# Performance work log

Measured on AMD Instinct MI355X. Metric: run time of the kernel, lower is better.

## Reference

```python
import jax, jax.numpy as jnp
import numpy as np

B = 128   # batch_size (number of trees / source tweets)
H = 100   # tweet_out_size == GRU hidden == GAT feature dim


def _gru_layer(x, h0, Wih, Whh, bih, bhh):
    # x: [T, N, D] time-major; PyTorch GRU cell math
    def step(h, xt):
        gi = xt @ Wih.T + bih
        gh = h @ Whh.T + bhh
        ir, iz, in_ = jnp.split(gi, 3, axis=-1)
        hr, hz, hn = jnp.split(gh, 3, axis=-1)
        r = jax.nn.sigmoid(ir + hr)
        z = jax.nn.sigmoid(iz + hz)
        n = jnp.tanh(in_ + r * hn)
        h = (1.0 - z) * n + z * h
        return h, h
    hT, ys = jax.lax.scan(step, h0, x)
    return ys, hT


def _gru2(x, h0, Wih0, Whh0, bih0, bhh0, Wih1, Whh1, bih1, bhh1):
    y0, _ = _gru_layer(x, h0[0], Wih0, Whh0, bih0, bhh0)
    _, h1 = _gru_layer(y0, h0[1], Wih1, Whh1, bih1, bhh1)
    return h1  # final hidden of top layer: [N, H]


def _gat(x, ei, W, a_src, a_dst, b, heads, outc, concat):
    # PyG GATConv (eval mode, add_self_loops=True, leaky_relu slope 0.2)
    N = x.shape[0]
    loops = jnp.arange(N, dtype=ei.dtype)
    src = jnp.concatenate([ei[0], loops])
    dst = jnp.concatenate([ei[1], loops])
    h = (x @ W.T).reshape(N, heads, outc)           # [N, H, C]
    es = (h * a_src).sum(-1)                         # [N, H]
    ed = (h * a_dst).sum(-1)
    e = jax.nn.leaky_relu(es[src] + ed[dst], negative_slope=0.2)  # [E, H]
    m = jax.lax.stop_gradient(jax.ops.segment_max(e, dst, num_segments=N))
    ee = jnp.exp(e - m[dst])
    s = jax.ops.segment_sum(ee, dst, num_segments=N)
    alpha = ee / s[dst]
    out = jax.ops.segment_sum(h[src] * alpha[:, :, None], dst, num_segments=N)
    out = out.reshape(N, heads * outc) if concat else out.mean(axis=1)
    return out + b


def _forward(fl, user_text, gnode, gei, tnode, tei, idx):
    (user_feats, h0g, h0t, temb,
     gWih0, gWhh0, gbih0, gbhh0, gWih1, gWhh1, gbih1, gbhh1,
     tWih0, tWhh0, tbih0, tbhh0, tWih1, tWhh1, tbih1, tbhh1,
     uW1, ub1, uW2, ub2,
     gc1W, gc1as, gc1ad, gc1b, gc2W, gc2as, gc2ad, gc2b,
     tc1W, tc1as, tc1ad, tc1b, tc2W, tc2as, tc2ad, tc2b,
     fcW, fcb) = fl
    # --- graphGAT branch ---
    ue = jax.nn.relu(user_feats @ uW1.T + ub1) @ uW2.T + ub2        # [Nu, 100]
    ge = temb[gnode].transpose(1, 0, 2)                              # [T, Ntg, 100]
    hg = _gru2(ge, h0g, gWih0, gWhh0, gbih0, gbhh0, gWih1, gWhh1, gbih1, gbhh1)
    xg = jnp.concatenate([hg[:B], ue, hg[B:]], axis=0)               # [Ng, 100]
    xg = jax.nn.relu(_gat(xg, gei, gc1W, gc1as, gc1ad, gc1b, 8, 64, True))
    xg = jax.nn.relu(_gat(xg, gei, gc2W, gc2as, gc2ad, gc2b, 1, 100, False))
    # --- TreeGAT branch ---
    te = temb[tnode].transpose(1, 0, 2)                              # [T, Ntree, 100]
    ht = _gru2(te, h0t, tWih0, tWhh0, tbih0, tbhh0, tWih1, tWhh1, tbih1, tbhh1)
    xt = ht.at[:B].set(xg[:B])                                       # root rows <- user_root_embed
    xt = jax.nn.relu(_gat(xt, tei, tc1W, tc1as, tc1ad, tc1b, 8, 100, True))
    xt = jax.nn.relu(_gat(xt, tei, tc2W, tc2as, tc2ad, tc2b, 1, 100, False))
    # --- scatter_mean over trees + classifier ---
    ssum = jax.ops.segment_sum(xt, idx, num_segments=B)
    cnt = jax.ops.segment_sum(jnp.ones((xt.shape[0],), xt.dtype), idx, num_segments=B)
    mean = ssum / jnp.maximum(cnt, 1.0)[:, None]
    return mean @ fcW.T + fcb                                        # [B, 4]


def setup_inputs():
    key = jax.random.key(0)
    it = iter(jax.random.split(key, 60))
    def nrm(shape, s):
        return (jax.random.normal(next(it), shape) * s).astype(jnp.float32)
    Ntg, Nu, Ntree = 10000, 20000, 30000
    Ng = Ntg + Nu
    Eg, Et, V, T = 200000, 60000, 50000, 20
    inp = {}
    inp["user_text"] = jax.random.randint(next(it), (Nu, 10), 0, 1000)
    inp["user_feats"] = nrm((Nu, 9), 1.0)
    inp["graph_node_features"] = jax.random.randint(next(it), (Ntg, T), 0, V)
    inp["graph_edge_index"] = jax.random.randint(next(it), (2, Eg), 0, Ng)
    inp["merged_tree_feature"] = jax.random.randint(next(it), (Ntree, T), 0, V)
    inp["merged_tree_edge_index"] = jax.random.randint(next(it), (2, Et), 0, Ntree)
    inp["indices"] = jax.random.randint(next(it), (Ntree,), 0, B)
    inp["h0_graph"] = nrm((2, Ntg, H), 1.0)
    inp["h0_tree"] = nrm((2, Ntree, H), 1.0)
    inp["tweet_emb"] = nrm((V, H), 1.0)
    s = 0.1
    for p in ("g", "t"):
        for l in ("0", "1"):
            inp[p + "Wih" + l] = nrm((3 * H, H), s)
            inp[p + "Whh" + l] = nrm((3 * H, H), s)
            inp[p + "bih" + l] = jnp.zeros((3 * H,), jnp.float32)
            inp[p + "bhh" + l] = jnp.zeros((3 * H,), jnp.float32)
    inp["uW1"] = nrm((100, 9), s);    inp["ub1"] = jnp.zeros((100,), jnp.float32)
    inp["uW2"] = nrm((100, 100), s);  inp["ub2"] = jnp.zeros((100,), jnp.float32)
    inp["gc1W"] = nrm((512, 100), s); inp["gc1as"] = nrm((8, 64), s); inp["gc1ad"] = nrm((8, 64), s); inp["gc1b"] = jnp.zeros((512,), jnp.float32)
    inp["gc2W"] = nrm((100, 512), s); inp["gc2as"] = nrm((1, 100), s); inp["gc2ad"] = nrm((1, 100), s); inp["gc2b"] = jnp.zeros((100,), jnp.float32)
    inp["tc1W"] = nrm((800, 100), s); inp["tc1as"] = nrm((8, 100), s); inp["tc1ad"] = nrm((8, 100), s); inp["tc1b"] = jnp.zeros((800,), jnp.float32)
    inp["tc2W"] = nrm((100, 800), s); inp["tc2as"] = nrm((1, 100), s); inp["tc2ad"] = nrm((1, 100), s); inp["tc2b"] = jnp.zeros((100,), jnp.float32)
    inp["fcW"] = nrm((4, 100), s);    inp["fcb"] = jnp.zeros((4,), jnp.float32)
    return inp


def reference(user_text, user_feats, graph_node_features, graph_edge_index,
              merged_tree_feature, merged_tree_edge_index, indices,
              h0_graph, h0_tree, tweet_emb,
              gWih0, gWhh0, gbih0, gbhh0, gWih1, gWhh1, gbih1, gbhh1,
              tWih0, tWhh0, tbih0, tbhh0, tWih1, tWhh1, tbih1, tbhh1,
              uW1, ub1, uW2, ub2,
              gc1W, gc1as, gc1ad, gc1b, gc2W, gc2as, gc2ad, gc2b,
              tc1W, tc1as, tc1ad, tc1b, tc2W, tc2as, tc2ad, tc2b,
              fcW, fcb):
    fl = (user_feats, h0_graph, h0_tree, tweet_emb,
          gWih0, gWhh0, gbih0, gbhh0, gWih1, gWhh1, gbih1, gbhh1,
          tWih0, tWhh0, tbih0, tbhh0, tWih1, tWhh1, tbih1, tbhh1,
          uW1, ub1, uW2, ub2,
          gc1W, gc1as, gc1ad, gc1b, gc2W, gc2as, gc2ad, gc2b,
          tc1W, tc1as, tc1ad, tc1b, tc2W, tc2as, tc2ad, tc2b,
          fcW, fcb)
    return _forward(fl, user_text, graph_node_features, graph_edge_index,
                    merged_tree_feature, merged_tree_edge_index, indices)
```

## Files before the change

### kernel.cpp

```cpp
#include <hip/hip_runtime.h>

#define NB    128
#define HD    100
#define NU    20000
#define NTG   10000
#define NTREE 30000
#define NG    30000
#define TT    20
#define EG    200000
#define ET    60000
#define VOC   50000

#define ESTR2 448
#define WROWS 336
#define LOG2E  1.4426950408889634f
#define LOG2E2 2.8853900817779268f

typedef unsigned short u16;
typedef unsigned int   u32;
typedef __attribute__((ext_vector_type(8))) short short8;
typedef __attribute__((ext_vector_type(4))) float floatx4;

__device__ __forceinline__ float sigmoid2_(float y) {
    return __fdividef(1.f, 1.f + __builtin_amdgcn_exp2f(-y));
}
__device__ __forceinline__ float tanh2_(float y) {
    return 1.f - __fdividef(2.f, __builtin_amdgcn_exp2f(y) + 1.f);
}
__device__ __forceinline__ u16 f2bf(float f) {
    u32 u = __float_as_uint(f);
    u32 r = (u + 0x7fffu + ((u >> 16) & 1u)) >> 16;
    return (u16)r;
}
__device__ __forceinline__ u16 f2bf_c(float f) {
    u32 r;
    asm("v_cvt_pk_bf16_f32 %0, %1, %2" : "=v"(r) : "v"(f), "v"(f));
    return (u16)r;
}
__device__ __forceinline__ float bf2f(u16 h) {
    return __uint_as_float(((u32)h) << 16);
}

struct GruProb {
    const u16*   Etab;
    const int*   nodes;
    const float* h0;
    const u16*   Whh0;
    const u16*   Wih1;
    const u16*   Whh1;
    u16*         hout;
    int          M;
};

__global__ __launch_bounds__(448, 2) void gru_fused10(GruProb Pg, GruProb Pt, int gblocks)
{
    const bool isg = (int)blockIdx.x < gblocks;
    const GruProb P = isg ? Pg : Pt;
    const int bx = isg ? blockIdx.x : blockIdx.x - gblocks;
    const int M  = P.M;
    const int m0 = bx * 32;

    __shared__ u16 H0[2][32 * 128];
    __shared__ u16 H1[2][32 * 128];
    __shared__ int NID[TT * 32];

    const int tid  = threadIdx.x;
    const int w    = tid >> 6, lane = tid & 63;
    const int fr   = lane & 15, quad = lane >> 4;
    const int c    = w * 16 + fr;
    const bool cok = (c < HD);

    short8 Bh0[3][4], Bx1[3][4], Bh1[3][4];
#pragma unroll
    for (int g = 0; g < 3; ++g) {
        const size_t rb = (size_t)((g * 7 + w) * 16 + fr) * 128 + quad * 8;
#pragma unroll
        for (int kk = 0; kk < 4; ++kk) {
            Bh0[g][kk] = *(const short8*)(P.Whh0 + rb + kk * 32);
            Bx1[g][kk] = *(const short8*)(P.Wih1 + rb + kk * 32);
            Bh1[g][kk] = *(const short8*)(P.Whh1 + rb + kk * 32);
        }
    }

    for (int i = tid; i < 32 * 128; i += 448) {
        H0[0][i] = 0; H0[1][i] = 0; H1[0][i] = 0; H1[1][i] = 0;
    }
    for (int i = tid; i < 32 * TT; i += 448) {
        int row = i / TT, t = i - row * TT;
        int gm = m0 + row;
        NID[t * 32 + row] = (gm < M) ? P.nodes[(size_t)gm * TT + t] : 0;
    }
    __syncthreads();
    if (tid < 32) {
        int off = 200 ^ ((tid & 7) << 4);
        *(u16*)((char*)&H0[0][0] + tid * 256 + off) = 0x3F80;
        *(u16*)((char*)&H0[1][0] + tid * 256 + off) = 0x3F80;
        *(u16*)((char*)&H1[0][0] + tid * 256 + off) = 0x3F80;
// ... 254 lines not shown
            acc[t] = __builtin_amdgcn_mfma_f32_16x16x32_bf16(af, bf, acc[t], 0, 0, 0);
        }
    }

    const int orow0 = m0 + (wave << 4) + quad * 4;
#pragma unroll
    for (int t = 0; t < 4; ++t) {
        int col = n0 + (t << 4) + fr;
        if (col >= N) continue;
#pragma unroll
        for (int r = 0; r < 4; ++r)
            Cb[(size_t)(orow0 + r) * ESTR2 + col] = f2bf(acc[t][r]);
    }
}

__global__ __launch_bounds__(256) void gemm_nt(
    const float* __restrict__ A, const float* __restrict__ W,
    const float* __restrict__ bias, float* __restrict__ C,
    int M, int N, int K, int relu)
{
    const int m0 = blockIdx.x * 64;
    const int n0 = blockIdx.y * 64;
    __shared__ float As[20][68];
    __shared__ float Ws[20][68];
    const int tid = threadIdx.x;
    const int r0 = (tid >> 4) * 4;
    const int c0 = (tid & 15) * 4;
    int sr[5], sk[5];
#pragma unroll
    for (int it = 0; it < 5; ++it) {
        int idx = tid + it * 256;
        sr[it] = idx / 20; sk[it] = idx - sr[it] * 20;
    }
    float acc[4][4];
#pragma unroll
    for (int i = 0; i < 4; ++i)
#pragma unroll
        for (int j = 0; j < 4; ++j) acc[i][j] = 0.f;
    const int nch = (K + 19) / 20;
    for (int ch = 0; ch < nch; ++ch) {
        const int k0 = ch * 20;
#pragma unroll
        for (int it = 0; it < 5; ++it) {
            int m = m0 + sr[it], k = k0 + sk[it];
            float va = 0.f, vw = 0.f;
            if (k < K) {
                if (m < M) va = A[(size_t)m * K + k];
                int n = n0 + sr[it];
                if (n < N) vw = W[(size_t)n * K + k];
            }
            As[sk[it]][sr[it]] = va;
            Ws[sk[it]][sr[it]] = vw;
        }
        __syncthreads();
#pragma unroll
        for (int kkk = 0; kkk < 20; ++kkk) {
            float4 a = *(const float4*)&As[kkk][r0];
            float4 w = *(const float4*)&Ws[kkk][c0];
            float av[4] = {a.x, a.y, a.z, a.w};
            float wv[4] = {w.x, w.y, w.z, w.w};
#pragma unroll
            for (int i = 0; i < 4; ++i)
#pragma unroll
                for (int j = 0; j < 4; ++j)
                    acc[i][j] = fmaf(av[i], wv[j], acc[i][j]);
        }
        __syncthreads();
    }
#pragma unroll
    for (int i = 0; i < 4; ++i) {
        int m = m0 + r0 + i;
        if (m >= M) continue;
#pragma unroll
        for (int j = 0; j < 4; ++j) {
            int n = n0 + c0 + j;
            if (n >= N) continue;
            float v = acc[i][j] + (bias ? bias[n] : 0.f);
            if (relu) v = fmaxf(v, 0.f);
            C[(size_t)m * N + n] = v;
        }
    }
}

__global__ void convert_pad2(const float* __restrict__ src, u16* __restrict__ dst,
                             int M, int Mp, int K, int ldk,
                             const float* __restrict__ app, int appone)
{
    int t = blockIdx.x * blockDim.x + threadIdx.x;
    if (t >= Mp * ldk) return;
    int n = t / ldk, c = t - n * ldk;
    u16 o = 0;
    if (n < M) {
        if (c < K) o = f2bf(src[(size_t)n * K + c]);
        else if (c == 100) {
            if (app) o = f2bf(app[n]);
            else if (appone) o = 0x3F80;
        }
    }
    dst[t] = o;
}

struct CvtgBatch {
    const float* src[6];
    const float* bias[6];
    u16*         dst[6];
};
#define CVTG_BLOCKS_PER_MAT 168
__global__ void convert_gru_w6(CvtgBatch B)
{
    int mat = blockIdx.x / CVTG_BLOCKS_PER_MAT;
    int t = (blockIdx.x - mat * CVTG_BLOCKS_PER_MAT) * blockDim.x + threadIdx.x;
    int rr = t >> 7, cc = t & 127;
    int g = rr / 112, r2 = rr - g * 112;
    u16 o = 0;
    if (r2 < 100) {
        float sc = (g == 2) ? LOG2E2 : LOG2E;
        int sr = g * 100 + r2;
        if (cc < 100) o = f2bf(B.src[mat][(size_t)sr * 100 + cc] * sc);
        else if (cc == 100) o = f2bf(B.bias[mat][sr] * sc);
    }
    B.dst[mat][t] = o;
}

__global__ void convert_ih0(const float* __restrict__ s0, const float* __restrict__ b0,
                            u16* __restrict__ d0,
                            const float* __restrict__ s1, const float* __restrict__ b1,
                            u16* __restrict__ d1)
{
    int t = blockIdx.x * blockDim.x + threadIdx.x;
    if (t >= 2 * 448 * 128) return;
    int which = t / (448 * 128);
    int tt = t - which * (448 * 128);
    const float* s = which ? s1 : s0;
    const float* b = which ? b1 : b0;
    u16* d = which ? d1 : d0;
    int j = tt >> 7, kc = tt & 127;
    int cc = j >> 2, g = j & 3;
    u16 o = 0;
    if (g < 3 && cc < 100) {
        float sc = (g == 2) ? LOG2E2 : LOG2E;
        int sr = g * 100 + cc;
        if (kc < 100) o = f2bf(s[(size_t)sr * 100 + kc] * sc);
        else if (kc == 100) o = f2bf(b[sr] * sc);
    }
    d[tt] = o;
}

__global__ void build_xg_bf(const u16* __restrict__ hgb, const float* __restrict__ ue,
                            u16* __restrict__ xgb)
{
    int t = blockIdx.x * blockDim.x + threadIdx.x;
    if (t >= NG * 128) return;
    int n = t >> 7, c = t & 127;
    u16 o = 0;
    if (n < NB)           o = hgb[n * 128 + c];
    else if (n < NB + NU) { if (c < HD) o = f2bf(ue[(size_t)(n - NB) * HD + c]); }
    else                  o = hgb[(size_t)(n - NU) * 128 + c];
    xgb[t] = o;
}

__global__ void set_roots(const float* __restrict__ src, u16* __restrict__ hb)
{
    int t = blockIdx.x * blockDim.x + threadIdx.x;
    if (t >= NB * HD) return;
    int n = t / HD, c = t - n * HD;
    hb[(size_t)n * 128 + c] = f2bf(src[t]);
}

__global__ void csr_count2(const int* __restrict__ gei, const int* __restrict__ tei,
                           int* __restrict__ gcnt, int* __restrict__ tcnt)
{
    int e = blockIdx.x * blockDim.x + threadIdx.x;
    const int GE = EG + NG;
    if (e < GE) {
        int dst = (e < EG) ? gei[EG + e] : e - EG;
        atomicAdd(&gcnt[dst], 1);
    } else {
        int e2 = e - GE;
        if (e2 >= ET + NTREE) return;
        int dst = (e2 < ET) ? tei[ET + e2] : e2 - ET;
        atomicAdd(&tcnt[dst], 1);
    }
}

__global__ void csr_scan2(int* __restrict__ gcnt, int* __restrict__ goff, int* __restrict__ gcur,
                          int* __restrict__ tcnt, int* __restrict__ toff, int* __restrict__ tcur)
{
    const int* cnt = blockIdx.x ? tcnt : gcnt;
    int* off = blockIdx.x ? toff : goff;
    int* cur = blockIdx.x ? tcur : gcur;
    const int N = blockIdx.x ? NTREE : NG;
    __shared__ int part[256];
    const int tid = threadIdx.x;
    const int per = (N + 255) / 256;
    const int i0 = tid * per;
    const int i1 = min(i0 + per, N);
    int s = 0;
    for (int i = i0; i < i1; ++i) s += cnt[i];
    part[tid] = s;
    __syncthreads();
    for (int o = 1; o < 256; o <<= 1) {
        int u = (tid >= o) ? part[tid - o] : 0;
        __syncthreads();
        part[tid] += u;
        __syncthreads();
    }
    int base = part[tid] - s;
    for (int i = i0; i < i1; ++i) {
        off[i] = base; cur[i] = base;
        base += cnt[i];
    }
    if (tid == 255) off[N] = part[255];
}

__global__ void csr_scatter2(const int* __restrict__ gei, const int* __restrict__ tei,
                             int* __restrict__ gcur, int* __restrict__ tcur,
                             int* __restrict__ geidx, int* __restrict__ teidx)
{
    int e = blockIdx.x * blockDim.x + threadIdx.x;
    const int GE = EG + NG;
    if (e < GE) {
        int dst = (e < EG) ? gei[EG + e] : e - EG;
        int pos = atomicAdd(&gcur[dst], 1);
        geidx[pos] = e;
    } else {
        int e2 = e - GE;
        if (e2 >= ET + NTREE) return;
        int dst = (e2 < ET) ? tei[ET + e2] : e2 - ET;
        int pos = atomicAdd(&tcur[dst], 1);
        teidx[pos] = e2;
    }
}

__global__ void gat_es_ed(const u16* __restrict__ feat, const float* __restrict__ asrc,
                          const float* __restrict__ adst, float* __restrict__ es,
                          float* __restrict__ ed, int N, int heads, int C)
{
    int gid = blockIdx.x * blockDim.x + threadIdx.x;
    if (gid >= N * heads) return;
    int n = gid / heads, hd = gid - n * heads;
    const u16* hp = feat + ((size_t)n * heads + hd) * C;
    const float* as = asrc + (size_t)hd * C;
    const float* ad = adst + (size_t)hd * C;
    float s1 = 0.f, s2 = 0.f;
    for (int c = 0; c < C; c += 4) {
        uint2 pk = *(const uint2*)(hp + c);
        float v0 = bf2f((u16)(pk.x & 0xffff)), v1 = bf2f((u16)(pk.x >> 16));
        float v2 = bf2f((u16)(pk.y & 0xffff)), v3 = bf2f((u16)(pk.y >> 16));
        s1 += v0 * as[c] + v1 * as[c + 1] + v2 * as[c + 2] + v3 * as[c + 3];
        s2 += v0 * ad[c] + v1 * ad[c + 1] + v2 * ad[c + 2] + v3 * ad[c + 3];
    }
    es[gid] = s1; ed[gid] = s2;
}

template<int HEADS>
__global__ __launch_bounds__(256) void gat_alpha_csr(
    const int* __restrict__ off, const int* __restrict__ eidx,
    const int* __restrict__ ei, int E,
    const float* __restrict__ es, const float* __restrict__ ed,
    float* __restrict__ eb, int N)
{
    int gt = blockIdx.x * blockDim.x + threadIdx.x;
    int dst = gt >> 6, lane = gt & 63;
    if (dst >= N) return;
    const int hd  = lane & (HEADS - 1);
    const int esl = lane / HEADS;
    const int EPI = 64 / HEADS;
    const int e0 = off[dst], e1 = off[dst + 1];
    const float edv = ed[(size_t)dst * HEADS + hd];

    float mymax = -3.4e38f;
    for (int p0 = e0; p0 < e1; p0 += EPI) {
        int p = p0 + esl;
        if (p < e1) {
            int j = eidx[p];
            int src = (j < E) ? ei[j] : (j - E);
            float e = es[(size_t)src * HEADS + hd] + edv;
            e = e > 0.f ? e : 0.2f * e;
            mymax = fmaxf(mymax, e);
        }
    }
#pragma unroll
    for (int o = HEADS; o < 64; o <<= 1)
        mymax = fmaxf(mymax, __shfl_xor(mymax, o));

    float ssum = 0.f;
    for (int p0 = e0; p0 < e1; p0 += EPI) {
        int p = p0 + esl;
        if (p < e1) {
            int j = eidx[p];
            int src = (j < E) ? ei[j] : (j - E);
            float e = es[(size_t)src * HEADS + hd] + edv;
            e = e > 0.f ? e : 0.2f * e;
            ssum += __expf(e - mymax);
        }
    }
#pragma unroll
    for (int o = HEADS; o < 64; o <<= 1)
        ssum += __shfl_xor(ssum, o);
    float sinv = __fdividef(1.f, ssum);

    for (int p0 = e0; p0 < e1; p0 += EPI) {
        int p = p0 + esl;
        if (p < e1) {
            int j = eidx[p];
            int src = (j < E) ? ei[j] : (j - E);
            float e = es[(size_t)src * HEADS + hd] + edv;
            e = e > 0.f ? e : 0.2f * e;
            eb[(size_t)j * HEADS + hd] = __expf(e - mymax) * sinv;
        }
    }
}

template<int C, int VEC>
__global__ __launch_bounds__(256) void gat_accum_csr(
    const int* __restrict__ off, const int* __restrict__ eidx,
    const int* __restrict__ ei, int E,
    const float* __restrict__ eb,
    const u16* __restrict__ feat, const float* __restrict__ bias,
    float* __restrict__ outf, u16* __restrict__ outb,
    int N, int heads, int HC, int nchunk)
{
    int gt = blockIdx.x * blockDim.x + threadIdx.x;
    int w = gt >> 6, lane = gt & 63;
    int dst = w / nchunk, chunk = w - dst * nchunk;
    if (dst >= N) return;
    int c0 = chunk * 64 * VEC + lane * VEC;
    if (c0 >= HC) return;
    int hh[VEC]; float acc[VEC];
#pragma unroll
    for (int v = 0; v < VEC; ++v) {
        int c = c0 + v;
        hh[v] = c / C;
        acc[v] = 0.f;
    }
    int e0 = off[dst], e1 = off[dst + 1];
    for (int p = e0; p < e1; ++p) {
        int j = eidx[p];
        int src = (j < E) ? ei[j] : (j - E);
        const u16* frp = feat + (size_t)src * HC + c0;
        float fv[VEC];
        if (VEC == 8) {
            uint4 pk = *(const uint4*)frp;
            fv[0] = bf2f((u16)(pk.x & 0xffff)); fv[1] = bf2f((u16)(pk.x >> 16));
            fv[2] = bf2f((u16)(pk.y & 0xffff)); fv[3] = bf2f((u16)(pk.y >> 16));
            fv[4] = bf2f((u16)(pk.z & 0xffff)); fv[5] = bf2f((u16)(pk.z >> 16));
            fv[6] = bf2f((u16)(pk.w & 0xffff)); fv[7] = bf2f((u16)(pk.w >> 16));
        } else if (VEC == 4) {
            uint2 pk = *(const uint2*)frp;
            fv[0] = bf2f((u16)(pk.x & 0xffff)); fv[1] = bf2f((u16)(pk.x >> 16));
            fv[2] = bf2f((u16)(pk.y & 0xffff)); fv[3] = bf2f((u16)(pk.y >> 16));
        } else {
            u32 pk = *(const u32*)frp;
            fv[0] = bf2f((u16)(pk & 0xffff)); fv[1] = bf2f((u16)(pk >> 16));
        }
#pragma unroll
        for (int v = 0; v < VEC; ++v)
            acc[v] += fv[v] * eb[(size_t)j * heads + hh[v]];
    }
#pragma unroll
    for (int v = 0; v < VEC; ++v) {
        int c = c0 + v;
        if (c >= HC) continue;
        float o = fmaxf(acc[v] + bias[c], 0.f);
        if (outf) outf[(size_t)dst * HC + c] = o;
        if (outb) outb[(size_t)dst * HC + c] = f2bf(o);
    }
}

__global__ void scatter_mean_accum(const float* __restrict__ x, const int* __restrict__ idx,
                                   float* __restrict__ ssum, float* __restrict__ cnt)
{
    int t = blockIdx.x * blockDim.x + threadIdx.x;
    if (t >= NTREE * HD) return;
    int n = t / HD, c = t - n * HD;
    int b = idx[n];
    atomicAdd(&ssum[b * HD + c], x[t]);
    if (c == 0) atomicAdd(&cnt[b], 1.f);
}

__global__ void fc_out(const float* __restrict__ ssum, const float* __restrict__ cnt,
                       const float* __restrict__ W, const float* __restrict__ b,
                       float* __restrict__ out)
{
    int t = threadIdx.x;
    int bb = t >> 2, j = t & 3;
    float inv = __fdividef(1.f, fmaxf(cnt[bb], 1.f));
    float acc = b[j];
    for (int k = 0; k < HD; ++k) acc += ssum[bb * HD + k] * inv * W[j * HD + k];
    out[t] = acc;
}

extern "C" void kernel_launch(void* const* d_in, const int* in_sizes, int n_in,
                              void* d_out, int out_size, void* d_ws, size_t ws_size,
                              hipStream_t stream)
{
    const float* user_feats = (const float*)d_in[1];
    const int*   gnf        = (const int*)d_in[2];
    const int*   gei        = (const int*)d_in[3];
    const int*   tnf        = (const int*)d_in[4];
    const int*   tei        = (const int*)d_in[5];
    const int*   indices    = (const int*)d_in[6];
    const float* h0g        = (const float*)d_in[7];
    const float* h0t        = (const float*)d_in[8];
    const float* temb       = (const float*)d_in[9];
    const float* gW[2][4] = {{(const float*)d_in[10], (const float*)d_in[11], (const float*)d_in[12], (const float*)d_in[13]},
                             {(const float*)d_in[14], (const float*)d_in[15], (const float*)d_in[16], (const float*)d_in[17]}};
    const float* tW[2][4] = {{(const float*)d_in[18], (const float*)d_in[19], (const float*)d_in[20], (const float*)d_in[21]},
                             {(const float*)d_in[22], (const float*)d_in[23], (const float*)d_in[24], (const float*)d_in[25]}};
    const float* uW1 = (const float*)d_in[26]; const float* ub1 = (const float*)d_in[27];
    const float* uW2 = (const float*)d_in[28]; const float* ub2 = (const float*)d_in[29];
    const float* gc1W = (const float*)d_in[30]; const float* gc1as = (const float*)d_in[31];
    const float* gc1ad = (const float*)d_in[32]; const float* gc1b = (const float*)d_in[33];
    const float* gc2W = (const float*)d_in[34]; const float* gc2as = (const float*)d_in[35];
    const float* gc2ad = (const float*)d_in[36]; const float* gc2b = (const float*)d_in[37];
    const float* tc1W = (const float*)d_in[38]; const float* tc1as = (const float*)d_in[39];
    const float* tc1ad = (const float*)d_in[40]; const float* tc1b = (const float*)d_in[41];
    const float* tc2W = (const float*)d_in[42]; const float* tc2as = (const float*)d_in[43];
    const float* tc2ad = (const float*)d_in[44]; const float* tc2b = (const float*)d_in[45];
    const float* fcW = (const float*)d_in[46]; const float* fcb = (const float*)d_in[47];
    float* out = (float*)d_out;

    char* ws = (char*)d_ws;
    const size_t NEED = 226500000;
    if (ws_size < NEED) return;

    float* XGF    = (float*)(ws + 0);
    u16*   TEMB_B = (u16*)(ws + 12000000);
    u16*   ETAB_G = (u16*)(ws + 25000000);
    u16*   ETAB_T = (u16*)(ws + 70000000);
    u16*   GH1B   = (u16*)(ws + 115000000);
    u16*   TH1B   = (u16*)(ws + 117600000);
    float* UE     = (float*)(ws + 125300000);
    float* HID    = (float*)(ws + 133400000);
    u16*   WARENA = (u16*)(ws + 141500000);
    int*   GOFF   = (int*)(ws + 142700000);
    int*   GCUR   = (int*)(ws + 142900000);
    int*   GCNT   = (int*)(ws + 143100000);
    int*   TCNT   = (int*)(ws + 143220000);
    int*   GEIDX  = (int*)(ws + 143400000);
    int*   TOFF   = (int*)(ws + 144400000);
    int*   TCUR   = (int*)(ws + 144600000);
    int*   TEIDX  = (int*)(ws + 144800000);
    float* ESB    = (float*)(ws + 145300000);
    float* EDB    = (float*)(ws + 146300000);
    float* EBB    = (float*)(ws + 149300000);
    float* SSUM   = (float*)(ws + 156700000);
    float* SCNT   = (float*)(ws + 156800000);
    u16*   XG_B   = (u16*)(ws + 157000000);
    u16*   GFEAT1 = (u16*)(ws + 165000000);
    u16*   GOUT1B = (u16*)(ws + 25000000);
    u16*   GFEAT2 = (u16*)(ws + 56000000);
    u16*   TFEAT1 = (u16*)(ws + 25000000);
    u16*   TOUT1B = (u16*)(ws + 74000000);
    u16*   TFEAT2 = (u16*)(ws + 123000000);
    float* XOUT2  = (float*)(ws + 157000000);

    u16* gWHH0  = WARENA + 0;
    u16* gWIH1  = WARENA + 43008;
    u16* gWHH1  = WARENA + 86016;
    u16* tWHH0  = WARENA + 129024;
    u16* tWIH1  = WARENA + 172032;
    u16* tWHH1  = WARENA + 215040;
    u16* W_IH0A = WARENA + 258048;
    u16* W_IH0B = WARENA + 315392;
    u16* W_G1   = WARENA + 372736;
    u16* W_G2   = WARENA + 475136;

    auto cvt = [&](const float* src, u16* dst, int M, int Mp, int K, int ldk,
                   const float* app = nullptr, int appone = 0) {
        convert_pad2<<<((size_t)Mp * ldk + 255) / 256, 256, 0, stream>>>(
            src, dst, M, Mp, K, ldk, app, appone);
    };
    auto mfma = [&](const u16* A, int lda, const u16* W, int ldw,
                    float* Cf, u16* Cb, int ldc, int M, int N, int Kt) {
        dim3 grid((M + 63) / 64, (N + 63) / 64, 1);
        gemm_mfma<<<grid, 256, 0, stream>>>(A, W, Cf, Cb, M, N, Kt, lda, ldw, ldc);
    };

    {
        dim3 g1((NU + 63) / 64, (HD + 63) / 64, 1);
        gemm_nt<<<g1, 256, 0, stream>>>(user_feats, uW1, ub1, HID, NU, HD, 9, 1);
        gemm_nt<<<g1, 256, 0, stream>>>(HID, uW2, ub2, UE, NU, HD, HD, 0);
    }

    cvt(temb, TEMB_B, VOC, VOC, HD, 128, nullptr, 1);
    {
        CvtgBatch B;
        B.src[0] = gW[0][1]; B.bias[0] = gW[0][3]; B.dst[0] = gWHH0;
        B.src[1] = gW[1][0]; B.bias[1] = gW[1][2]; B.dst[1] = gWIH1;
        B.src[2] = gW[1][1]; B.bias[2] = gW[1][3]; B.dst[2] = gWHH1;
        B.src[3] = tW[0][1]; B.bias[3] = tW[0][3]; B.dst[3] = tWHH0;
        B.src[4] = tW[1][0]; B.bias[4] = tW[1][2]; B.dst[4] = tWIH1;
        B.src[5] = tW[1][1]; B.bias[5] = tW[1][3]; B.dst[5] = tWHH1;
        convert_gru_w6<<<6 * CVTG_BLOCKS_PER_MAT, 256, 0, stream>>>(B);
    }
    convert_ih0<<<(2 * 448 * 128 + 255) / 256, 256, 0, stream>>>(
        gW[0][0], gW[0][2], W_IH0A, tW[0][0], tW[0][2], W_IH0B);
    {
        dim3 ge((VOC + 63) / 64, 7, 2);
        gemm_etab<<<ge, 256, 0, stream>>>(TEMB_B, W_IH0A, W_IH0B, ETAB_G, ETAB_T);
    }

    hipMemsetAsync(GCNT, 0, 143400000 - 143100000, stream);
    {
        int tot = (EG + NG) + (ET + NTREE);
        csr_count2<<<(tot + 255) / 256, 256, 0, stream>>>(gei, tei, GCNT, TCNT);
        csr_scan2<<<2, 256, 0, stream>>>(GCNT, GOFF, GCUR, TCNT, TOFF, TCUR);
        csr_scatter2<<<(tot + 255) / 256, 256, 0, stream>>>(gei, tei, GCUR, TCUR, GEIDX, TEIDX);
    }

    {
        GruProb Pg = { ETAB_G, gnf, h0g, gWHH0, gWIH1, gWHH1, GH1B, NTG };
        GruProb Pt = { ETAB_T, tnf, h0t, tWHH0, tWIH1, tWHH1, TH1B, NTREE };
        int gblk = (NTG + 31) / 32;
        int tblk = (NTREE + 31) / 32;
        gru_fused10<<<gblk + tblk, 448, 0, stream>>>(Pg, Pt, gblk);
    }

    build_xg_bf<<<(NG * 128 + 255) / 256, 256, 0, stream>>>(GH1B, UE, XG_B);
    cvt(gc1W, W_G1, 512, 512, HD, 128);
    cvt(gc2W, W_G2, 100, 100, 512, 512);
    {
        mfma(XG_B, 128, W_G1, 128, nullptr, GFEAT1, 512, NG, 512, 4);
        gat_es_ed<<<(NG * 8 + 255) / 256, 256, 0, stream>>>(GFEAT1, gc1as, gc1ad, ESB, EDB, NG, 8, 64);
        gat_alpha_csr<8><<<(NG + 3) / 4, 256, 0, stream>>>(GOFF, GEIDX, gei, EG, ESB, EDB, EBB, NG);
        gat_accum_csr<64, 8><<<(NG + 3) / 4, 256, 0, stream>>>(
            GOFF, GEIDX, gei, EG, EBB, GFEAT1, gc1b, nullptr, GOUT1B, NG, 8, 512, 1);
    }
    {
        mfma(GOUT1B, 512, W_G2, 512, nullptr, GFEAT2, 100, NG, 100, 16);
        gat_es_ed<<<(NG + 255) / 256, 256, 0, stream>>>(GFEAT2, gc2as, gc2ad, ESB, EDB, NG, 1, 100);
        gat_alpha_csr<1><<<(NG + 3) / 4, 256, 0, stream>>>(GOFF, GEIDX, gei, EG, ESB, EDB, EBB, NG);
        gat_accum_csr<100, 2><<<(NG + 3) / 4, 256, 0, stream>>>(
            GOFF, GEIDX, gei, EG, EBB, GFEAT2, gc2b, XGF, nullptr, NG, 1, 100, 1);
    }

    set_roots<<<(NB * HD + 255) / 256, 256, 0, stream>>>(XGF, TH1B);
    cvt(tc1W, W_G1, 800, 800, HD, 128);
    cvt(tc2W, W_G2, 100, 100, 800, 800);
    {
        mfma(TH1B, 128, W_G1, 128, nullptr, TFEAT1, 800, NTREE, 800, 4);
        gat_es_ed<<<(NTREE * 8 + 255) / 256, 256, 0, stream>>>(TFEAT1, tc1as, tc1ad, ESB, EDB, NTREE, 8, 100);
        gat_alpha_csr<8><<<(NTREE + 3) / 4, 256, 0, stream>>>(TOFF, TEIDX, tei, ET, ESB, EDB, EBB, NTREE);
        gat_accum_csr<100, 8><<<(NTREE * 2 + 3) / 4, 256, 0, stream>>>(
            TOFF, TEIDX, tei, ET, EBB, TFEAT1, tc1b, nullptr, TOUT1B, NTREE, 8, 800, 2);
    }
    {
        mfma(TOUT1B, 800, W_G2, 800, nullptr, TFEAT2, 100, NTREE, 100, 25);
        gat_es_ed<<<(NTREE + 255) / 256, 256, 0, stream>>>(TFEAT2, tc2as, tc2ad, ESB, EDB, NTREE, 1, 100);
        gat_alpha_csr<1><<<(NTREE + 3) / 4, 256, 0, stream>>>(TOFF, TEIDX, tei, ET, ESB, EDB, EBB, NTREE);
        gat_accum_csr<100, 2><<<(NTREE + 3) / 4, 256, 0, stream>>>(
            TOFF, TEIDX, tei, ET, EBB, TFEAT2, tc2b, XOUT2, nullptr, NTREE, 1, 100, 1);
    }

    hipMemsetAsync(SSUM, 0, (size_t)NB * HD * 4, stream);
    hipMemsetAsync(SCNT, 0, (size_t)NB * 4, stream);
    scatter_mean_accum<<<(NTREE * HD + 255) / 256, 256, 0, stream>>>(XOUT2, indices, SSUM, SCNT);
    fc_out<<<1, 512, 0, stream>>>(SSUM, SCNT, fcW, fcb, out);
}
```

Before: 1.485 ms.

## Fuse GAT alpha into aggregation, batch weight conversions, CSR-based scatter mean

```diff
diff --git a/kernel.cpp b/kernel.cpp
--- a/kernel.cpp
+++ b/kernel.cpp
@@ -12,7 +12,6 @@
 #define VOC   50000
 
 #define ESTR2 448
-#define WROWS 336
 #define LOG2E  1.4426950408889634f
 #define LOG2E2 2.8853900817779268f
 
@@ -433,68 +432,74 @@
     }
 }
 
-__global__ void convert_pad2(const float* __restrict__ src, u16* __restrict__ dst,
-                             int M, int Mp, int K, int ldk,
-                             const float* __restrict__ app, int appone)
-{
-    int t = blockIdx.x * blockDim.x + threadIdx.x;
-    if (t >= Mp * ldk) return;
+struct CvtAll {
+    const float* temb;  u16* tembB;
+    const float* gsrc[6]; const float* gbias[6]; u16* gdst[6];
+    const float* is[2];   const float* ib[2];    u16* id_[2];
+    const float* wsrc[4]; u16* wdst[4];
+    int wK[4]; int wLdk[4]; int wTot[4];
+};
+#define CB_TEMB 25000
+#define CB_GRUW 168
+#define CB_IH0  224
+#define CB_WTOT 1169
+
+__global__ void convert_all(CvtAll P)
+{
+    int b = blockIdx.x;
+    const int tid = threadIdx.x;
+    if (b < CB_TEMB) {
+        int t = b * 256 + tid;
+        int n = t >> 7, c = t & 127;
+        u16 o = 0;
+        if (c < 100) o = f2bf(P.temb[(size_t)n * 100 + c]);
+        else if (c == 100) o = 0x3F80;
+        P.tembB[t] = o;
+        return;
+    }
+    b -= CB_TEMB;
+    if (b < 6 * CB_GRUW) {
+        int mat = b / CB_GRUW;
+        int t = (b - mat * CB_GRUW) * 256 + tid;
+        int rr = t >> 7, cc = t & 127;
+        int g = rr / 112, r2 = rr - g * 112;
+        u16 o = 0;
+        if (r2 < 100) {
+            float sc = (g == 2) ? LOG2E2 : LOG2E;
+            int sr = g * 100 + r2;
+            if (cc < 100) o = f2bf(P.gsrc[mat][(size_t)sr * 100 + cc] * sc);
+            else if (cc == 100) o = f2bf(P.gbias[mat][sr] * sc);
+        }
+        P.gdst[mat][t] = o;
+        return;
+    }
+    b -= 6 * CB_GRUW;
+    if (b < 2 * CB_IH0) {
+        int which = b / CB_IH0;
+        int t = (b - which * CB_IH0) * 256 + tid;
+        int j = t >> 7, kc = t & 127;
+        int cc = j >> 2, g = j & 3;
+        u16 o = 0;
+        if (g < 3 && cc < 100) {
+            float sc = (g == 2) ? LOG2E2 : LOG2E;
+            int sr = g * 100 + cc;
+            if (kc < 100) o = f2bf(P.is[which][(size_t)sr * 100 + kc] * sc);
+            else if (kc == 100) o = f2bf(P.ib[which][sr] * sc);
+        }
+        P.id_[which][t] = o;
+        return;
+    }
+    b -= 2 * CB_IH0;
+    int seg, t;
+    if (b < 256)      { seg = 0; t = b * 256 + tid; }
+    else if (b < 456) { seg = 1; t = (b - 256) * 256 + tid; }
+    else if (b < 856) { seg = 2; t = (b - 456) * 256 + tid; }
+    else              { seg = 3; t = (b - 856) * 256 + tid; }
+    if (t >= P.wTot[seg]) return;
+    int K = P.wK[seg], ldk = P.wLdk[seg];
     int n = t / ldk, c = t - n * ldk;
-    u16 o = 0;
-    if (n < M) {
-        if (c < K) o = f2bf(src[(size_t)n * K + c]);
-        else if (c == 100) {
-            if (app) o = f2bf(app[n]);
-            else if (appone) o = 0x3F80;
-        }
-    }
-    dst[t] = o;
-}
-
-struct CvtgBatch {
-    const float* src[6];
-    const float* bias[6];
-    u16*         dst[6];
-};
-#define CVTG_BLOCKS_PER_MAT 168
-__global__ void convert_gru_w6(CvtgBatch B)
-{
-    int mat = blockIdx.x / CVTG_BLOCKS_PER_MAT;
-    int t = (blockIdx.x - mat * CVTG_BLOCKS_PER_MAT) * blockDim.x + threadIdx.x;
-    int rr = t >> 7, cc = t & 127;
-    int g = rr / 112, r2 = rr - g * 112;
-    u16 o = 0;
-    if (r2 < 100) {
-        float sc = (g == 2) ? LOG2E2 : LOG2E;
-        int sr = g * 100 + r2;
-        if (cc < 100) o = f2bf(B.src[mat][(size_t)sr * 100 + cc] * sc);
-        else if (cc == 100) o = f2bf(B.bias[mat][sr] * sc);
-    }
-    B.dst[mat][t] = o;
-}
-
-__global__ void convert_ih0(const float* __restrict__ s0, const float* __restrict__ b0,
-                            u16* __restrict__ d0,
-                            const float* __restrict__ s1, const float* __restrict__ b1,
-                            u16* __restrict__ d1)
-{
-    int t = blockIdx.x * blockDim.x + threadIdx.x;
-    if (t >= 2 * 448 * 128) return;
-    int which = t / (448 * 128);
-    int tt = t - which * (448 * 128);
-    const float* s = which ? s1 : s0;
-    const float* b = which ? b1 : b0;
-    u16* d = which ? d1 : d0;
-    int j = tt >> 7, kc = tt & 127;
-    int cc = j >> 2, g = j & 3;
-    u16 o = 0;
-    if (g < 3 && cc < 100) {
-        float sc = (g == 2) ? LOG2E2 : LOG2E;
-        int sr = g * 100 + cc;
-        if (kc < 100) o = f2bf(s[(size_t)sr * 100 + kc] * sc);
-        else if (kc == 100) o = f2bf(b[sr] * sc);
-    }
-    d[tt] = o;
+    u16 o = (c < K) ? f2bf(P.wsrc[seg][(size_t)n * K + c]) : (u16)0;
+    P.wdst[seg][t] = o;
 }
 
 __global__ void build_xg_bf(const u16* __restrict__ hgb, const float* __restrict__ ue,
@@ -519,28 +524,34 @@
 }
 
 __global__ void csr_count2(const int* __restrict__ gei, const int* __restrict__ tei,
-                           int* __restrict__ gcnt, int* __restrict__ tcnt)
+                           const int* __restrict__ bmap,
+                           int* __restrict__ gcnt, int* __restrict__ tcnt,
+                           int* __restrict__ bcnt)
 {
     int e = blockIdx.x * blockDim.x + threadIdx.x;
-    const int GE = EG + NG;
+    const int GE = EG + NG, TE = ET + NTREE;
     if (e < GE) {
         int dst = (e < EG) ? gei[EG + e] : e - EG;
         atomicAdd(&gcnt[dst], 1);
-    } else {
+    } else if (e < GE + TE) {
         int e2 = e - GE;
-        if (e2 >= ET + NTREE) return;
         int dst = (e2 < ET) ? tei[ET + e2] : e2 - ET;
         atomicAdd(&tcnt[dst], 1);
+    } else {
+        int e3 = e - GE - TE;
+        if (e3 >= NTREE) return;
+        atomicAdd(&bcnt[bmap[e3]], 1);
     }
 }
 
 __global__ void csr_scan2(int* __restrict__ gcnt, int* __restrict__ goff, int* __restrict__ gcur,
-                          int* __restrict__ tcnt, int* __restrict__ toff, int* __restrict__ tcur)
-{
-    const int* cnt = blockIdx.x ? tcnt : gcnt;
-    int* off = blockIdx.x ? toff : goff;
-    int* cur = blockIdx.x ? tcur : gcur;
-    const int N = blockIdx.x ? NTREE : NG;
+                          int* __restrict__ tcnt, int* __restrict__ toff, int* __restrict__ tcur,
+                          int* __restrict__ bcnt, int* __restrict__ boff, int* __restrict__ bcur)
+{
+    const int* cnt; int* off; int* cur; int N;
+    if (blockIdx.x == 0)      { cnt = gcnt; off = goff; cur = gcur; N = NG; }
+    else if (blockIdx.x == 1) { cnt = tcnt; off = toff; cur = tcur; N = NTREE; }
+    else                      { cnt = bcnt; off = boff; cur = bcur; N = NB; }
     __shared__ int part[256];
     const int tid = threadIdx.x;
     const int per = (N + 255) / 256;
@@ -565,21 +576,28 @@
 }
 
 __global__ void csr_scatter2(const int* __restrict__ gei, const int* __restrict__ tei,
+                             const int* __restrict__ bmap,
                              int* __restrict__ gcur, int* __restrict__ tcur,
-                             int* __restrict__ geidx, int* __restrict__ teidx)
+                             int* __restrict__ bcur,
+                             int* __restrict__ geidx, int* __restrict__ teidx,
+                             int* __restrict__ bidx)
 {
     int e = blockIdx.x * blockDim.x + threadIdx.x;
-    const int GE = EG + NG;
+    const int GE = EG + NG, TE = ET + NTREE;
     if (e < GE) {
         int dst = (e < EG) ? gei[EG + e] : e - EG;
         int pos = atomicAdd(&gcur[dst], 1);
         geidx[pos] = e;
-    } else {
+    } else if (e < GE + TE) {
         int e2 = e - GE;
-        if (e2 >= ET + NTREE) return;
         int dst = (e2 < ET) ? tei[ET + e2] : e2 - ET;
         int pos = atomicAdd(&tcur[dst], 1);
         teidx[pos] = e2;
+    } else {
+        int e3 = e - GE - TE;
+        if (e3 >= NTREE) return;
+        int pos = atomicAdd(&bcur[bmap[e3]], 1);
+        bidx[pos] = e3;
     }
 }
 
@@ -604,91 +622,75 @@
     es[gid] = s1; ed[gid] = s2;
 }
 
-template<int HEADS>
-__global__ __launch_bounds__(256) void gat_alpha_csr(
+template<int C, int VEC, int HEADS, int NCHUNK>
+__global__ __launch_bounds__(256) void gat_fused(
     const int* __restrict__ off, const int* __restrict__ eidx,
     const int* __restrict__ ei, int E,
     const float* __restrict__ es, const float* __restrict__ ed,
-    float* __restrict__ eb, int N)
+    const u16* __restrict__ feat, const float* __restrict__ bias,
+    float* __restrict__ outf, u16* __restrict__ outb,
+    int N, int HC)
 {
     int gt = blockIdx.x * blockDim.x + threadIdx.x;
-    int dst = gt >> 6, lane = gt & 63;
+    int wid = gt >> 6, lane = gt & 63;
+    int dst = wid / NCHUNK, chunk = wid - dst * NCHUNK;
     if (dst >= N) return;
+    const int e0 = off[dst], e1 = off[dst + 1];
+
     const int hd  = lane & (HEADS - 1);
     const int esl = lane / HEADS;
     const int EPI = 64 / HEADS;
-    const int e0 = off[dst], e1 = off[dst + 1];
-    const float edv = ed[(size_t)dst * HEADS + hd];
+    float edv = ed[(size_t)dst * HEADS + hd];
 
     float mymax = -3.4e38f;
-    for (int p0 = e0; p0 < e1; p0 += EPI) {
-        int p = p0 + esl;
-        if (p < e1) {
-            int j = eidx[p];
-            int src = (j < E) ? ei[j] : (j - E);
-            float e = es[(size_t)src * HEADS + hd] + edv;
-            e = e > 0.f ? e : 0.2f * e;
-            mymax = fmaxf(mymax, e);
-        }
+    for (int p = e0 + esl; p < e1; p += EPI) {
+        int j = eidx[p];
+        int src = (j < E) ? ei[j] : (j - E);
+        float e = es[(size_t)src * HEADS + hd] + edv;
+        e = e > 0.f ? e : 0.2f * e;
+        mymax = fmaxf(mymax, e);
     }
 #pragma unroll
     for (int o = HEADS; o < 64; o <<= 1)
         mymax = fmaxf(mymax, __shfl_xor(mymax, o));
 
     float ssum = 0.f;
-    for (int p0 = e0; p0 < e1; p0 += EPI) {
-        int p = p0 + esl;
-        if (p < e1) {
-            int j = eidx[p];
-            int src = (j < E) ? ei[j] : (j - E);
-            float e = es[(size_t)src * HEADS + hd] + edv;
-            e = e > 0.f ? e : 0.2f * e;
-            ssum += __expf(e - mymax);
-        }
+    for (int p = e0 + esl; p < e1; p += EPI) {
+        int j = eidx[p];
+        int src = (j < E) ? ei[j] : (j - E);
+        float e = es[(size_t)src * HEADS + hd] + edv;
+        e = e > 0.f ? e : 0.2f * e;
+        ssum += __expf(e - mymax);
     }
 #pragma unroll
     for (int o = HEADS; o < 64; o <<= 1)
         ssum += __shfl_xor(ssum, o);
     float sinv = __fdividef(1.f, ssum);
 
-    for (int p0 = e0; p0 < e1; p0 += EPI) {
-        int p = p0 + esl;
-        if (p < e1) {
-            int j = eidx[p];
-            int src = (j < E) ? ei[j] : (j - E);
-            float e = es[(size_t)src * HEADS + hd] + edv;
-            e = e > 0.f ? e : 0.2f * e;
-            eb[(size_t)j * HEADS + hd] = __expf(e - mymax) * sinv;
-        }
-    }
-}
-
-template<int C, int VEC>
-__global__ __launch_bounds__(256) void gat_accum_csr(
-    const int* __restrict__ off, const int* __restrict__ eidx,
-    const int* __restrict__ ei, int E,
-    const float* __restrict__ eb,
-    const u16* __restrict__ feat, const float* __restrict__ bias,
-    float* __restrict__ outf, u16* __restrict__ outb,
-    int N, int heads, int HC, int nchunk)
-{
-    int gt = blockIdx.x * blockDim.x + threadIdx.x;
-    int w = gt >> 6, lane = gt & 63;
-    int dst = w / nchunk, chunk = w - dst * nchunk;
-    if (dst >= N) return;
     int c0 = chunk * 64 * VEC + lane * VEC;
+    int split = (c0 / C + 1) * C - c0;
+    int hlo = c0 / C;              if (hlo > HEADS - 1) hlo = HEADS - 1;
+    int hhi = (c0 + VEC - 1) / C;  if (hhi > HEADS - 1) hhi = HEADS - 1;
+    float maxlo = __shfl(mymax, hlo), sinvlo = __shfl(sinv, hlo), edlo = __shfl(edv, hlo);
+    float maxhi = __shfl(mymax, hhi), sinvhi = __shfl(sinv, hhi), edhi = __shfl(edv, hhi);
+
     if (c0 >= HC) return;
-    int hh[VEC]; float acc[VEC];
-#pragma unroll
-    for (int v = 0; v < VEC; ++v) {
-        int c = c0 + v;
-        hh[v] = c / C;
-        acc[v] = 0.f;
-    }
-    int e0 = off[dst], e1 = off[dst + 1];
+    float acc[VEC];
+#pragma unroll
+    for (int v = 0; v < VEC; ++v) acc[v] = 0.f;
+
     for (int p = e0; p < e1; ++p) {
         int j = eidx[p];
         int src = (j < E) ? ei[j] : (j - E);
+        float elo = es[(size_t)src * HEADS + hlo] + edlo;
+        elo = elo > 0.f ? elo : 0.2f * elo;
+        float alo = __expf(elo - maxlo) * sinvlo;
+        float ahi = alo;
+        if (hhi != hlo) {
+            float ehi = es[(size_t)src * HEADS + hhi] + edhi;
+            ehi = ehi > 0.f ? ehi : 0.2f * ehi;
+            ahi = __expf(ehi - maxhi) * sinvhi;
+        }
         const u16* frp = feat + (size_t)src * HC + c0;
         float fv[VEC];
         if (VEC == 8) {
@@ -697,17 +699,15 @@
             fv[2] = bf2f((u16)(pk.y & 0xffff)); fv[3] = bf2f((u16)(pk.y >> 16));
             fv[4] = bf2f((u16)(pk.z & 0xffff)); fv[5] = bf2f((u16)(pk.z >> 16));
             fv[6] = bf2f((u16)(pk.w & 0xffff)); fv[7] = bf2f((u16)(pk.w >> 16));
-        } else if (VEC == 4) {
-            uint2 pk = *(const uint2*)frp;
-            fv[0] = bf2f((u16)(pk.x & 0xffff)); fv[1] = bf2f((u16)(pk.x >> 16));
-            fv[2] = bf2f((u16)(pk.y & 0xffff)); fv[3] = bf2f((u16)(pk.y >> 16));
         } else {
             u32 pk = *(const u32*)frp;
             fv[0] = bf2f((u16)(pk & 0xffff)); fv[1] = bf2f((u16)(pk >> 16));
         }
 #pragma unroll
-        for (int v = 0; v < VEC; ++v)
-            acc[v] += fv[v] * eb[(size_t)j * heads + hh[v]];
+        for (int v = 0; v < VEC; ++v) {
+            float a = (v < split) ? alo : ahi;
+            acc[v] += fv[v] * a;
+        }
     }
 #pragma unroll
     for (int v = 0; v < VEC; ++v) {
@@ -719,26 +719,35 @@
     }
 }
 
-__global__ void scatter_mean_accum(const float* __restrict__ x, const int* __restrict__ idx,
-                                   float* __restrict__ ssum, float* __restrict__ cnt)
-{
-    int t = blockIdx.x * blockDim.x + threadIdx.x;
-    if (t >= NTREE * HD) return;
-    int n = t / HD, c = t - n * HD;
-    int b = idx[n];
-    atomicAdd(&ssum[b * HD + c], x[t]);
-    if (c == 0) atomicAdd(&cnt[b], 1.f);
-}
-
-__global__ void fc_out(const float* __restrict__ ssum, const float* __restrict__ cnt,
-                       const float* __restrict__ W, const float* __restrict__ b,
-                       float* __restrict__ out)
+__global__ void scatter_mean_csr(const int* __restrict__ boff, const int* __restrict__ bidx,
+                                 const float* __restrict__ x, float* __restrict__ meanb)
+{
+    int b = blockIdx.x;
+    int tid = threadIdx.x;
+    int c = tid & 127, half = tid >> 7;
+    __shared__ float partial[256];
+    int i0 = boff[b], i1 = boff[b + 1];
+    float acc = 0.f;
+    if (c < HD) {
+        for (int i = i0 + half; i < i1; i += 2)
+            acc += x[(size_t)bidx[i] * HD + c];
+    }
+    partial[tid] = acc;
+    __syncthreads();
+    if (half == 0 && c < HD) {
+        float tot = partial[tid] + partial[tid + 128];
+        float cnt = (float)(i1 - i0);
+        meanb[b * HD + c] = tot * __fdividef(1.f, fmaxf(cnt, 1.f));
+    }
+}
+
+__global__ void fc_out2(const float* __restrict__ meanb, const float* __restrict__ W,
+                        const float* __restrict__ b, float* __restrict__ out)
 {
     int t = threadIdx.x;
     int bb = t >> 2, j = t & 3;
-    float inv = __fdividef(1.f, fmaxf(cnt[bb], 1.f));
     float acc = b[j];
-    for (int k = 0; k < HD; ++k) acc += ssum[bb * HD + k] * inv * W[j * HD + k];
+    for (int k = 0; k < HD; ++k) acc += meanb[bb * HD + k] * W[j * HD + k];
     out[t] = acc;
 }
 
@@ -789,17 +798,23 @@
     int*   GCUR   = (int*)(ws + 142900000);
     int*   GCNT   = (int*)(ws + 143100000);
     int*   TCNT   = (int*)(ws + 143220000);
+    int*   BCNT   = (int*)(ws + 143340000);
     int*   GEIDX  = (int*)(ws + 143400000);
     int*   TOFF   = (int*)(ws + 144400000);
     int*   TCUR   = (int*)(ws + 144600000);
     int*   TEIDX  = (int*)(ws + 144800000);
+    int*   BOFF   = (int*)(ws + 145160000);
+    int*   BCUR   = (int*)(ws + 145170000);
+    int*   BIDX   = (int*)(ws + 145180000);
     float* ESB    = (float*)(ws + 145300000);
     float* EDB    = (float*)(ws + 146300000);
-    float* EBB    = (float*)(ws + 149300000);
-    float* SSUM   = (float*)(ws + 156700000);
-    float* SCNT   = (float*)(ws + 156800000);
+    float* MEANB  = (float*)(ws + 156700000);
     u16*   XG_B   = (u16*)(ws + 157000000);
     u16*   GFEAT1 = (u16*)(ws + 165000000);
+    u16*   W_G1a  = (u16*)(ws + 196000000);
+    u16*   W_G2a  = (u16*)(ws + 196131072);
+    u16*   W_G1b  = (u16*)(ws + 196233472);
+    u16*   W_G2b  = (u16*)(ws + 196438272);
     u16*   GOUT1B = (u16*)(ws + 25000000);
     u16*   GFEAT2 = (u16*)(ws + 56000000);
     u16*   TFEAT1 = (u16*)(ws + 25000000);
@@ -815,14 +830,7 @@
     u16* tWHH1  = WARENA + 215040;
     u16* W_IH0A = WARENA + 258048;
     u16* W_IH0B = WARENA + 315392;
-    u16* W_G1   = WARENA + 372736;
-    u16* W_G2   = WARENA + 475136;
-
-    auto cvt = [&](const float* src, u16* dst, int M, int Mp, int K, int ldk,
-                   const float* app = nullptr, int appone = 0) {
-        convert_pad2<<<((size_t)Mp * ldk + 255) / 256, 256, 0, stream>>>(
-            src, dst, M, Mp, K, ldk, app, appone);
-    };
+
     auto mfma = [&](const u16* A, int lda, const u16* W, int ldw,
                     float* Cf, u16* Cb, int ldc, int M, int N, int Kt) {
         dim3 grid((M + 63) / 64, (N + 63) / 64, 1);
@@ -830,35 +838,42 @@
     };
 
     {
+        CvtAll P;
+        P.temb = temb; P.tembB = TEMB_B;
+        P.gsrc[0] = gW[0][1]; P.gbias[0] = gW[0][3]; P.gdst[0] = gWHH0;
+        P.gsrc[1] = gW[1][0]; P.gbias[1] = gW[1][2]; P.gdst[1] = gWIH1;
+        P.gsrc[2] = gW[1][1]; P.gbias[2] = gW[1][3]; P.gdst[2] = gWHH1;
+        P.gsrc[3] = tW[0][1]; P.gbias[3] = tW[0][3]; P.gdst[3] = tWHH0;
+        P.gsrc[4] = tW[1][0]; P.gbias[4] = tW[1][2]; P.gdst[4] = tWIH1;
+        P.gsrc[5] = tW[1][1]; P.gbias[5] = tW[1][3]; P.gdst[5] = tWHH1;
+        P.is[0] = gW[0][0]; P.ib[0] = gW[0][2]; P.id_[0] = W_IH0A;
+        P.is[1] = tW[0][0]; P.ib[1] = tW[0][2]; P.id_[1] = W_IH0B;
+        P.wsrc[0] = gc1W; P.wdst[0] = W_G1a; P.wK[0] = 100; P.wLdk[0] = 128; P.wTot[0] = 512 * 128;
+        P.wsrc[1] = gc2W; P.wdst[1] = W_G2a; P.wK[1] = 512; P.wLdk[1] = 512; P.wTot[1] = 100 * 512;
+        P.wsrc[2] = tc1W; P.wdst[2] = W_G1b; P.wK[2] = 100; P.wLdk[2] = 128; P.wTot[2] = 800 * 128;
+        P.wsrc[3] = tc2W; P.wdst[3] = W_G2b; P.wK[3] = 800; P.wLdk[3] = 800; P.wTot[3] = 100 * 800;
+        int grid = CB_TEMB + 6 * CB_GRUW + 2 * CB_IH0 + CB_WTOT;
+        convert_all<<<grid, 256, 0, stream>>>(P);
+    }
+
+    {
+        dim3 ge((VOC + 63) / 64, 7, 2);
+        gemm_etab<<<ge, 256, 0, stream>>>(TEMB_B, W_IH0A, W_IH0B, ETAB_G, ETAB_T);
+    }
+
+    hipMemsetAsync(GCNT, 0, 240512, stream);
+    {
+        int tot = (EG + NG) + (ET + NTREE) + NTREE;
+        csr_count2<<<(tot + 255) / 256, 256, 0, stream>>>(gei, tei, indices, GCNT, TCNT, BCNT);
+        csr_scan2<<<3, 256, 0, stream>>>(GCNT, GOFF, GCUR, TCNT, TOFF, TCUR, BCNT, BOFF, BCUR);
+        csr_scatter2<<<(tot + 255) / 256, 256, 0, stream>>>(gei, tei, indices,
+                                                            GCUR, TCUR, BCUR, GEIDX, TEIDX, BIDX);
+    }
+
+    {
         dim3 g1((NU + 63) / 64, (HD + 63) / 64, 1);
         gemm_nt<<<g1, 256, 0, stream>>>(user_feats, uW1, ub1, HID, NU, HD, 9, 1);
         gemm_nt<<<g1, 256, 0, stream>>>(HID, uW2, ub2, UE, NU, HD, HD, 0);
-    }
-
-    cvt(temb, TEMB_B, VOC, VOC, HD, 128, nullptr, 1);
-    {
-        CvtgBatch B;
-        B.src[0] = gW[0][1]; B.bias[0] = gW[0][3]; B.dst[0] = gWHH0;
-        B.src[1] = gW[1][0]; B.bias[1] = gW[1][2]; B.dst[1] = gWIH1;
-        B.src[2] = gW[1][1]; B.bias[2] = gW[1][3]; B.dst[2] = gWHH1;
-        B.src[3] = tW[0][1]; B.bias[3] = tW[0][3]; B.dst[3] = tWHH0;
-        B.src[4] = tW[1][0]; B.bias[4] = tW[1][2]; B.dst[4] = tWIH1;
-        B.src[5] = tW[1][1]; B.bias[5] = tW[1][3]; B.dst[5] = tWHH1;
-        convert_gru_w6<<<6 * CVTG_BLOCKS_PER_MAT, 256, 0, stream>>>(B);
-    }
-    convert_ih0<<<(2 * 448 * 128 + 255) / 256, 256, 0, stream>>>(
-        gW[0][0], gW[0][2], W_IH0A, tW[0][0], tW[0][2], W_IH0B);
-    {
-        dim3 ge((VOC + 63) / 64, 7, 2);
-        gemm_etab<<<ge, 256, 0, stream>>>(TEMB_B, W_IH0A, W_IH0B, ETAB_G, ETAB_T);
-    }
-
-    hipMemsetAsync(GCNT, 0, 143400000 - 143100000, stream);
-    {
-        int tot = (EG + NG) + (ET + NTREE);
-        csr_count2<<<(tot + 255) / 256, 256, 0, stream>>>(gei, tei, GCNT, TCNT);
-        csr_scan2<<<2, 256, 0, stream>>>(GCNT, GOFF, GCUR, TCNT, TOFF, TCUR);
-        csr_scatter2<<<(tot + 255) / 256, 256, 0, stream>>>(gei, tei, GCUR, TCUR, GEIDX, TEIDX);
     }
 
     {
@@ -870,43 +885,33 @@
     }
 
     build_xg_bf<<<(NG * 128 + 255) / 256, 256, 0, stream>>>(GH1B, UE, XG_B);
-    cvt(gc1W, W_G1, 512, 512, HD, 128);
-    cvt(gc2W, W_G2, 100, 100, 512, 512);
     {
-        mfma(XG_B, 128, W_G1, 128, nullptr, GFEAT1, 512, NG, 512, 4);
+        mfma(XG_B, 128, W_G1a, 128, nullptr, GFEAT1, 512, NG, 512, 4);
         gat_es_ed<<<(NG * 8 + 255) / 256, 256, 0, stream>>>(GFEAT1, gc1as, gc1ad, ESB, EDB, NG, 8, 64);
-        gat_alpha_csr<8><<<(NG + 3) / 4, 256, 0, stream>>>(GOFF, GEIDX, gei, EG, ESB, EDB, EBB, NG);
-        gat_accum_csr<64, 8><<<(NG + 3) / 4, 256, 0, stream>>>(
-            GOFF, GEIDX, gei, EG, EBB, GFEAT1, gc1b, nullptr, GOUT1B, NG, 8, 512, 1);
+        gat_fused<64, 8, 8, 1><<<(NG + 3) / 4, 256, 0, stream>>>(
+            GOFF, GEIDX, gei, EG, ESB, EDB, GFEAT1, gc1b, nullptr, GOUT1B, NG, 512);
     }
     {
-        mfma(GOUT1B, 512, W_G2, 512, nullptr, GFEAT2, 100, NG, 100, 16);
+        mfma(GOUT1B, 512, W_G2a, 512, nullptr, GFEAT2, 100, NG, 100, 16);
         gat_es_ed<<<(NG + 255) / 256, 256, 0, stream>>>(GFEAT2, gc2as, gc2ad, ESB, EDB, NG, 1, 100);
-        gat_alpha_csr<1><<<(NG + 3) / 4, 256, 0, stream>>>(GOFF, GEIDX, gei, EG, ESB, EDB, EBB, NG);
-        gat_accum_csr<100, 2><<<(NG + 3) / 4, 256, 0, stream>>>(
-            GOFF, GEIDX, gei, EG, EBB, GFEAT2, gc2b, XGF, nullptr, NG, 1, 100, 1);
+        gat_fused<100, 2, 1, 1><<<(NG + 3) / 4, 256, 0, stream>>>(
+            GOFF, GEIDX, gei, EG, ESB, EDB, GFEAT2, gc2b, XGF, nullptr, NG, 100);
     }
 
     set_roots<<<(NB * HD + 255) / 256, 256, 0, stream>>>(XGF, TH1B);
-    cvt(tc1W, W_G1, 800, 800, HD, 128);
-    cvt(tc2W, W_G2, 100, 100, 800, 800);
     {
-        mfma(TH1B, 128, W_G1, 128, nullptr, TFEAT1, 800, NTREE, 800, 4);
+        mfma(TH1B, 128, W_G1b, 128, nullptr, TFEAT1, 800, NTREE, 800, 4);
         gat_es_ed<<<(NTREE * 8 + 255) / 256, 256, 0, stream>>>(TFEAT1, tc1as, tc1ad, ESB, EDB, NTREE, 8, 100);
-        gat_alpha_csr<8><<<(NTREE + 3) / 4, 256, 0, stream>>>(TOFF, TEIDX, tei, ET, ESB, EDB, EBB, NTREE);
-        gat_accum_csr<100, 8><<<(NTREE * 2 + 3) / 4, 256, 0, stream>>>(
-            TOFF, TEIDX, tei, ET, EBB, TFEAT1, tc1b, nullptr, TOUT1B, NTREE, 8, 800, 2);
+        gat_fused<100, 8, 8, 2><<<(NTREE * 2 + 3) / 4, 256, 0, stream>>>(
+            TOFF, TEIDX, tei, ET, ESB, EDB, TFEAT1, tc1b, nullptr, TOUT1B, NTREE, 800);
     }
     {
-        mfma(TOUT1B, 800, W_G2, 800, nullptr, TFEAT2, 100, NTREE, 100, 25);
+        mfma(TOUT1B, 800, W_G2b, 800, nullptr, TFEAT2, 100, NTREE, 100, 25);
         gat_es_ed<<<(NTREE + 255) / 256, 256, 0, stream>>>(TFEAT2, tc2as, tc2ad, ESB, EDB, NTREE, 1, 100);
-        gat_alpha_csr<1><<<(NTREE + 3) / 4, 256, 0, stream>>>(TOFF, TEIDX, tei, ET, ESB, EDB, EBB, NTREE);
-        gat_accum_csr<100, 2><<<(NTREE + 3) / 4, 256, 0, stream>>>(
-            TOFF, TEIDX, tei, ET, EBB, TFEAT2, tc2b, XOUT2, nullptr, NTREE, 1, 100, 1);
-    }
-
-    hipMemsetAsync(SSUM, 0, (size_t)NB * HD * 4, stream);
-    hipMemsetAsync(SCNT, 0, (size_t)NB * 4, stream);
-    scatter_mean_accum<<<(NTREE * HD + 255) / 256, 256, 0, stream>>>(XOUT2, indices, SSUM, SCNT);
-    fc_out<<<1, 512, 0, stream>>>(SSUM, SCNT, fcW, fcb, out);
-}
+        gat_fused<100, 2, 1, 1><<<(NTREE + 3) / 4, 256, 0, stream>>>(
+            TOFF, TEIDX, tei, ET, ESB, EDB, TFEAT2, tc2b, XOUT2, nullptr, NTREE, 100);
+    }
+
+    scatter_mean_csr<<<NB, 256, 0, stream>>>(BOFF, BIDX, XOUT2, MEANB);
+    fc_out2<<<1, 512, 0, stream>>>(MEANB, fcW, fcb, out);
+}
```

Result: faster. 1.440 ms (-3.0%).
